# Kernel tuning notes

Measured on AMD Instinct MI355X. Metric: run time of the kernel, lower is better.

Reference implementation:

```python
import jax, jax.numpy as jnp
import numpy as np

B, S, DIN, DOUT, H = 4, 2048, 512, 512, 8
DH = DOUT // H
EPS = 1e-5


def _conv_bn(x, conv_w, conv_b, bn_gamma, bn_beta, bn_mean, bn_var):
    # x: [B, S, DIN] -> permute to [B, DIN, S] like torch
    xc = jnp.transpose(x, (0, 2, 1))
    y = jax.lax.conv_general_dilated(
        xc, conv_w, window_strides=(1,), padding=[(3, 3)],
        dimension_numbers=('NCH', 'OIH', 'NCH'))  # [B, DOUT, S]
    y = y + conv_b[None, :, None]
    # BatchNorm1d in eval mode: normalize per channel with running stats
    inv = jax.lax.rsqrt(bn_var + EPS)
    y = (y - bn_mean[None, :, None]) * (inv * bn_gamma)[None, :, None] + bn_beta[None, :, None]
    return jnp.transpose(y, (0, 2, 1))  # back to [B, S, DOUT]


def setup_inputs() -> dict:
    key = jax.random.key(0)
    ks = jax.random.split(key, 4)
    return {
        'q': jax.random.normal(ks[0], (B, S, DIN), dtype=jnp.float32),
        'k': jax.random.normal(ks[1], (B, S, DIN), dtype=jnp.float32),
        'v': jax.random.normal(ks[2], (B, S, DIN), dtype=jnp.float32),
        'conv_w': jax.random.normal(ks[3], (DOUT, DIN, 7), dtype=jnp.float32) * 0.02,
        'conv_b': jnp.zeros((DOUT,), jnp.float32),
        'bn_gamma': jnp.ones((DOUT,), jnp.float32),
        'bn_beta': jnp.zeros((DOUT,), jnp.float32),
        'bn_mean': jnp.zeros((DOUT,), jnp.float32),
        'bn_var': jnp.ones((DOUT,), jnp.float32),
        'ln_gamma': jnp.ones((DOUT,), jnp.float32),
        'ln_beta': jnp.zeros((DOUT,), jnp.float32),
    }


def reference(q, k, v, conv_w, conv_b, bn_gamma, bn_beta, bn_mean, bn_var,
              ln_gamma, ln_beta):
    # shared conv+BN preproc applied to q, k, v, then split into heads [B,S,H,DH]
    qh = _conv_bn(q, conv_w, conv_b, bn_gamma, bn_beta, bn_mean, bn_var).reshape(B, S, H, DH)
    kh = _conv_bn(k, conv_w, conv_b, bn_gamma, bn_beta, bn_mean, bn_var).reshape(B, S, H, DH)
    vh = _conv_bn(v, conv_w, conv_b, bn_gamma, bn_beta, bn_mean, bn_var).reshape(B, S, H, DH)
    # full QK^T score matrix, scaled, softmax, times V (mask is None)
    scores = jnp.einsum('bqhd,bkhd->bhqk', qh, kh) * (1.0 / np.sqrt(DH).astype(np.float32))
    probs = jax.nn.softmax(scores, axis=-1)
    out = jnp.einsum('bhqk,bkhd->bqhd', probs, vh).reshape(B, S, DOUT)
    # dropout(p=0) is identity; final LayerNorm over feature dim
    mu = jnp.mean(out, axis=-1, keepdims=True)
    var = jnp.mean(jnp.square(out - mu), axis=-1, keepdims=True)
    return (out - mu) * jax.lax.rsqrt(var + EPS) * ln_gamma + ln_beta
```

## Files before the change

kernel.cpp:

```cpp
#include <hip/hip_runtime.h>
#include <hip/hip_bf16.h>


#define B_ 4
#define S_ 2048
#define DIN_ 512
#define DOUT_ 512
#define H_ 8
#define DH_ 64
#define EPS_ 1e-5f
#define SP_ 2054

using bf16x8 = __attribute__((ext_vector_type(8))) short;
using f32x4  = __attribute__((ext_vector_type(4))) float;

__device__ __forceinline__ unsigned short f2bf(float x) {
    union { float f; unsigned u; } v; v.f = x;
    unsigned r = v.u + 0x7FFF + ((v.u >> 16) & 1);
    return (unsigned short)(r >> 16);
}

__device__ __forceinline__ unsigned cvt2(float lo, float hi) {
    unsigned r;
    asm("v_cvt_pk_bf16_f32 %0, %1, %2" : "=v"(r) : "v"(lo), "v"(hi));
    return r;
}

__device__ __forceinline__ float fexp2(float x) {
    float r;
    asm("v_exp_f32 %0, %1" : "=v"(r) : "v"(x));
    return r;
}

typedef __attribute__((address_space(1))) const unsigned int GU32;
typedef __attribute__((address_space(3))) unsigned int LU32;
__device__ __forceinline__ void gl_lds16(const void* g, void* l) {
    __builtin_amdgcn_global_load_lds((GU32*)g, (LU32*)l, 16, 0, 0);
}

__global__ void cast_x(const float* __restrict__ q, const float* __restrict__ k,
                       const float* __restrict__ v, unsigned short* __restrict__ xb) {
    int i = blockIdx.x * 256 + threadIdx.x;
    int row = i >> 6;
    int cin = (i & 63) * 8;
    int tb = row / SP_;
    int pr = row - tb * SP_;
    int tensor = tb >> 2;
    int b = tb & 3;
    unsigned short* dst = xb + (size_t)row * DIN_ + cin;
    if (pr < 3 || pr >= SP_ - 3) {
        *reinterpret_cast<uint4*>(dst) = make_uint4(0, 0, 0, 0);
    } else {
        const float* src = (tensor == 0 ? q : (tensor == 1 ? k : v)) +
                           ((size_t)b * S_ + (pr - 3)) * DIN_ + cin;
        float4 a0 = *reinterpret_cast<const float4*>(src);
        float4 a1 = *reinterpret_cast<const float4*>(src + 4);
        uint4 o;
        o.x = cvt2(a0.x, a0.y); o.y = cvt2(a0.z, a0.w);
        o.z = cvt2(a1.x, a1.y); o.w = cvt2(a1.z, a1.w);
        *reinterpret_cast<uint4*>(dst) = o;
    }
}

__global__ void prep_w(const float* __restrict__ w, const float* __restrict__ cb,
                       const float* __restrict__ gamma, const float* __restrict__ beta,
                       const float* __restrict__ mean, const float* __restrict__ var,
                       unsigned short* __restrict__ w_eff, float* __restrict__ b_eff) {
    int gid = blockIdx.x * blockDim.x + threadIdx.x;
    if (gid < DOUT_) {
        float sc = gamma[gid] * rsqrtf(var[gid] + EPS_);
        b_eff[gid] = (cb[gid] - mean[gid]) * sc + beta[gid];
    }
    int total = 7 * DOUT_ * DIN_;
    for (int i = gid; i < total; i += gridDim.x * blockDim.x) {
        int t = i / (DOUT_ * DIN_);
        int rem = i - t * (DOUT_ * DIN_);
        int co = rem >> 9;
        int ci = rem & 511;
        float sc = gamma[co] * rsqrtf(var[co] + EPS_);
        w_eff[i] = f2bf(w[(co * DIN_ + ci) * 7 + t] * sc);
    }
}

__global__ __launch_bounds__(256, 2) void conv_bn(
        const unsigned short* __restrict__ xb,
        const unsigned short* __restrict__ w_eff,
        const float* __restrict__ b_eff,
        unsigned short* __restrict__ out3) {
    __shared__ alignas(16) unsigned short As[2][192 * 32];
    __shared__ alignas(16) unsigned short Bs[3][256 * 32];

    int orig = blockIdx.x;
    int bid = (orig & 7) * 48 + (orig >> 3);
    int tensor = bid >> 7;
    int rem = bid & 127;
    int batch = rem >> 5;
    int stile = (rem >> 1) & 15;
    int cotile = rem & 1;
    int s0 = stile * 128;
    int co0 = cotile * 256;

    const unsigned short* xp = xb + (size_t)(tensor * 4 + batch) * SP_ * DIN_;
    unsigned short* out = out3 + (size_t)tensor * (B_ * S_ * DOUT_) +
                          (size_t)batch * S_ * DOUT_;

    const int tid = threadIdx.x;
    const int l = tid & 63;
    const int wv = tid >> 6;
    const int g = l >> 4;
    const int c16 = l & 15;
    const int wrow = (wv >> 1) * 64;
    const int wcol = (wv & 1) * 128;

    const int dr4 = l >> 2;
    const int sch = ((l & 3) ^ (dr4 & 3)) << 3;

#define STAGE_A(cc, buf) do {                                                   \
        _Pragma("unroll")                                                       \
        for (int j = 0; j < 3; ++j) {                                           \
            int r0 = (wv * 3 + j) * 16;                                         \
            int rs = r0 + dr4; if (rs > 133) rs = 133;                          \
            gl_lds16(xp + (size_t)(s0 + rs) * DIN_ + (cc) * 32 + sch,           \
                     &As[buf][r0 * 32]);                                        \
        }                                                                       \
    } while (0)

#define STAGE_B(cc, t, buf) do {                                                \
        const unsigned short* wp = w_eff + (size_t)(t) * (DOUT_ * DIN_) +       \
                                   (cc) * 32;                                   \
        _Pragma("unroll")                                                       \
        for (int j = 0; j < 4; ++j) {                                           \
            int r0 = (wv * 4 + j) * 16;                                         \
            gl_lds16(wp + (size_t)(co0 + r0 + dr4) * DIN_ + sch,                \
                     &Bs[buf][r0 * 32]);                                        \
        }                                                                       \
    } while (0)

    f32x4 acc[4][8] = {};

    STAGE_A(0, 0);
    STAGE_B(0, 0, 0);
    int bcur = 0;

    for (int cc = 0; cc < 16; ++cc) {
        const int ca = cc & 1;
        for (int t = 0; t < 7; ++t) {
            int bnext = bcur + 1; if (bnext == 3) bnext = 0;
            if (t < 6) {
                STAGE_B(cc, t + 1, bnext);
                asm volatile("s_waitcnt vmcnt(4)" ::: "memory");
            } else if (cc < 15) {
                STAGE_B(cc + 1, 0, bnext);
                STAGE_A(cc + 1, ca ^ 1);
                asm volatile("s_waitcnt vmcnt(7)" ::: "memory");
            } else {
                asm volatile("s_waitcnt vmcnt(0)" ::: "memory");
            }
            __builtin_amdgcn_s_barrier();

            const unsigned short* Ab = &As[ca][0];
            const unsigned short* Bb = &Bs[bcur][0];
            bf16x8 af[4], bfv[8];
#pragma unroll
            for (int m = 0; m < 4; ++m) {
                int r = wrow + m * 16 + c16 + t;
                af[m] = *reinterpret_cast<const bf16x8*>(
                    &Ab[r * 32 + ((g ^ (r & 3)) << 3)]);
            }
#pragma unroll
            for (int n = 0; n < 8; ++n) {
                int rb = wcol + n * 16 + c16;
                bfv[n] = *reinterpret_cast<const bf16x8*>(
                    &Bb[rb * 32 + ((g ^ (rb & 3)) << 3)]);
            }
            __builtin_amdgcn_s_setprio(1);
#pragma unroll
            for (int m = 0; m < 4; ++m)
#pragma unroll
                for (int n = 0; n < 8; ++n)
                    acc[m][n] = __builtin_amdgcn_mfma_f32_16x16x32_bf16(
                        af[m], bfv[n], acc[m][n], 0, 0, 0);
            __builtin_amdgcn_s_setprio(0);
            bcur = bnext;
        }
    }

    float osc = (tensor == 0) ? 0.125f * 1.44269504f : 1.0f;
#pragma unroll
    for (int m = 0; m < 4; ++m) {
        int rowb = s0 + wrow + m * 16 + 4 * g;
#pragma unroll
        for (int n = 0; n < 8; ++n) {
            int col = co0 + wcol + n * 16 + c16;
            float be = b_eff[col];
#pragma unroll
            for (int ri = 0; ri < 4; ++ri)
                out[(size_t)(rowb + ri) * DOUT_ + col] =
                    f2bf((acc[m][n][ri] + be) * osc);
        }
    }
#undef STAGE_A
#undef STAGE_B
}

__global__ void transpose_v(const unsigned short* __restrict__ vh,
                            unsigned short* __restrict__ vt) {
    __shared__ alignas(16) unsigned short T[64 * 64];
    int bid = blockIdx.x;
    int stile = bid & 31;
    int bh = bid >> 5;
    int b = bh >> 3;
    int h = bh & 7;
    int s0 = stile * 64;
    const unsigned short* src = vh + ((size_t)b * S_ + s0) * DOUT_ + h * DH_;
    unsigned short* dst = vt + (size_t)bh * DH_ * S_ + s0;
    int tid = threadIdx.x;
#pragma unroll
    for (int it = 0; it < 2; ++it) {
        int idx = tid + it * 256;
        int s = idx >> 3, dhc = idx & 7;
        uint4 val = *reinterpret_cast<const uint4*>(&src[(size_t)s * DOUT_ + dhc * 8]);
        *reinterpret_cast<uint4*>(&T[s * 64 + ((dhc ^ (s & 7) ^ ((s >> 3) & 7)) << 3)]) = val;
    }
    __syncthreads();
#pragma unroll
    for (int it = 0; it < 2; ++it) {
        int idx = tid + it * 256;
        int dh = idx >> 3, sc = idx & 7;
        unsigned short tmp[8];
#pragma unroll
        for (int j = 0; j < 8; ++j) {
            int s = sc * 8 + j;
            tmp[j] = T[s * 64 + (((dh >> 3) ^ (s & 7) ^ ((s >> 3) & 7)) << 3) + (dh & 7)];
        }
        *reinterpret_cast<uint4*>(&dst[(size_t)dh * S_ + sc * 8]) =
            *reinterpret_cast<const uint4*>(tmp);
    }
}

__global__ __launch_bounds__(256, 4) void attn(const unsigned short* __restrict__ qh,
                     const unsigned short* __restrict__ kh,
                     const unsigned short* __restrict__ vt,
                     float* __restrict__ out) {
    __shared__ alignas(16) unsigned short Ks[2][64 * 64];
    __shared__ alignas(16) unsigned short Vs[2][64 * 64];

    const int tid = threadIdx.x;
    const int l = tid & 63;
    const int wv = tid >> 6;
    const int g = l >> 4;
    const int c16 = l & 15;

    const int bid = blockIdx.x;
    const int qt = bid & 31;
    const int bh = bid >> 5;
    const int b = bh >> 3;
    const int h = bh & 7;
    const int s0 = qt * 64;

    const unsigned short* qp = qh + (size_t)b * S_ * DOUT_ + h * DH_;
    const unsigned short* kp = kh + (size_t)b * S_ * DOUT_ + h * DH_;
    const unsigned short* vp = vt + (size_t)bh * DH_ * S_;

    bf16x8 qf[2];
    {
        int row = s0 + wv * 16 + c16;
        qf[0] = *reinterpret_cast<const bf16x8*>(&qp[(size_t)row * DOUT_ + 8 * g]);
        qf[1] = *reinterpret_cast<const bf16x8*>(&qp[(size_t)row * DOUT_ + 32 + 8 * g]);
    }

    const int l3 = l >> 3;
    const int kchunk8 = ((l & 7) ^ l3) * 8;

#define STAGE(kt, buf) do {                                                          \
        const unsigned short* kgp = kp + (size_t)(kt) * 64 * DOUT_;                  \
        const unsigned short* vgp = vp + (size_t)(kt) * 64;                          \
        _Pragma("unroll")                                                            \
        for (int i = 0; i < 2; ++i) {                                                \
            int K0 = wv * 16 + i * 8;                                                \
            gl_lds16(kgp + (size_t)(K0 + l3) * DOUT_ + kchunk8, &Ks[buf][K0 * 64]);  \
            gl_lds16(vgp + (size_t)(K0 + l3) * S_   + kchunk8, &Vs[buf][K0 * 64]);   \
        }                                                                            \
    } while (0)

    f32x4 oacc[4] = {};
    float mrow = -1e30f, lrow = 0.f;

    const int sA = ((l & 16) << 1) | c16;
    const int sB = sA + 16;
    const bool hi = (l & 32) != 0;

    STAGE(0, 0);

    const int NT = S_ / 64;
    for (int kt = 0; kt < NT; ++kt) {
        const int cur = kt & 1;
        if (kt + 1 < NT) {
            STAGE(kt + 1, 1 - cur);
            asm volatile("s_waitcnt vmcnt(4)" ::: "memory");
        } else {
            asm volatile("s_waitcnt vmcnt(0)" ::: "memory");
        }
        __builtin_amdgcn_s_barrier();

        const char* KsB = (const char*)&Ks[cur][0];
        f32x4 sf[4] = {};
#pragma unroll
        for (int kk = 0; kk < 2; ++kk) {
            bf16x8 kf[4];
#pragma unroll
            for (int n = 0; n < 4; ++n)
                kf[n] = *reinterpret_cast<const bf16x8*>(
                    KsB + (n * 16 + c16) * 128 + (((4 * kk + g) ^ (l & 7)) << 4));
            __builtin_amdgcn_s_setprio(1);
#pragma unroll
            for (int n = 0; n < 4; ++n)
                sf[n] = __builtin_amdgcn_mfma_f32_16x16x32_bf16(kf[n], qf[kk], sf[n], 0, 0, 0);
            __builtin_amdgcn_s_setprio(0);
        }

        float t0 = fmaxf(fmaxf(sf[0][0], sf[0][1]), fmaxf(sf[0][2], sf[0][3]));
        float t1 = fmaxf(fmaxf(sf[1][0], sf[1][1]), fmaxf(sf[1][2], sf[1][3]));
        float t2 = fmaxf(fmaxf(sf[2][0], sf[2][1]), fmaxf(sf[2][2], sf[2][3]));
        float t3 = fmaxf(fmaxf(sf[3][0], sf[3][1]), fmaxf(sf[3][2], sf[3][3]));
        float m0 = fmaxf(fmaxf(t0, t1), fmaxf(t2, t3));
        m0 = fmaxf(m0, __shfl_xor(m0, 16, 64));
        m0 = fmaxf(m0, __shfl_xor(m0, 32, 64));
        if (!__all(m0 <= mrow + 8.f)) {
            float mnew = fmaxf(mrow, m0);
            float corr = fexp2(mrow - mnew);
            mrow = mnew;
            lrow *= corr;
#pragma unroll
            for (int n = 0; n < 4; ++n) {
                oacc[n][0] *= corr; oacc[n][1] *= corr;
                oacc[n][2] *= corr; oacc[n][3] *= corr;
            }
        }
        unsigned pk[4][2];
        float rsn[4];
#pragma unroll
        for (int n = 0; n < 4; ++n) {
            float p0 = fexp2(sf[n][0] - mrow);
            float p1 = fexp2(sf[n][1] - mrow);
            float p2 = fexp2(sf[n][2] - mrow);
            float p3 = fexp2(sf[n][3] - mrow);
            rsn[n] = (p0 + p1) + (p2 + p3);
            pk[n][0] = cvt2(p0, p1);
            pk[n][1] = cvt2(p2, p3);
        }
        float rs = (rsn[0] + rsn[1]) + (rsn[2] + rsn[3]);
        rs += __shfl_xor(rs, 16, 64);
        rs += __shfl_xor(rs, 32, 64);
        lrow += rs;

        const char* VsB = (const char*)&Vs[cur][0];
#pragma unroll
        for (int kk = 0; kk < 2; ++kk) {
            unsigned a0 = __shfl((int)pk[2 * kk][0], sA, 64);
            unsigned a1 = __shfl((int)pk[2 * kk][1], sA, 64);
            unsigned a2 = __shfl((int)pk[2 * kk][0], sB, 64);
            unsigned a3 = __shfl((int)pk[2 * kk][1], sB, 64);
            unsigned b0 = __shfl((int)pk[2 * kk + 1][0], sA, 64);
            unsigned b1 = __shfl((int)pk[2 * kk + 1][1], sA, 64);
            unsigned b2 = __shfl((int)pk[2 * kk + 1][0], sB, 64);
            unsigned b3 = __shfl((int)pk[2 * kk + 1][1], sB, 64);
            union { unsigned w[4]; bf16x8 v; } pu;
            pu.w[0] = hi ? b0 : a0;
            pu.w[1] = hi ? b1 : a1;
            pu.w[2] = hi ? b2 : a2;
            pu.w[3] = hi ? b3 : a3;
            bf16x8 vfr[4];
#pragma unroll
            for (int n = 0; n < 4; ++n)
                vfr[n] = *reinterpret_cast<const bf16x8*>(
                    VsB + (n * 16 + c16) * 128 + (((4 * kk + g) ^ (l & 7)) << 4));
            __builtin_amdgcn_s_setprio(1);
#pragma unroll
            for (int n = 0; n < 4; ++n)
                oacc[n] = __builtin_amdgcn_mfma_f32_16x16x32_bf16(vfr[n], pu.v, oacc[n], 0, 0, 0);
            __builtin_amdgcn_s_setprio(0);
        }
        __builtin_amdgcn_s_barrier();
    }

    {
        int row = s0 + wv * 16 + c16;
        float inv = 1.0f / lrow;
        float* op = out + (size_t)b * S_ * DOUT_ + h * DH_ + (size_t)row * DOUT_;
#pragma unroll
        for (int n = 0; n < 4; ++n) {
            f32x4 o = oacc[n];
            o[0] *= inv; o[1] *= inv; o[2] *= inv; o[3] *= inv;
            *reinterpret_cast<f32x4*>(&op[n * 16 + 4 * g]) = o;
        }
    }
#undef STAGE
}

__global__ void lnorm(float* __restrict__ out, const float* __restrict__ gamma,
                      const float* __restrict__ beta) {
    int tid = threadIdx.x;
    int lane = tid & 63;
    int wv = tid >> 6;
    int row = blockIdx.x * 4 + wv;
    float* p = out + (size_t)row * DOUT_;
    float4 v0 = *reinterpret_cast<const float4*>(&p[lane * 8]);
    float4 v1 = *reinterpret_cast<const float4*>(&p[lane * 8 + 4]);
    float s = v0.x + v0.y + v0.z + v0.w + v1.x + v1.y + v1.z + v1.w;
    float sq = v0.x * v0.x + v0.y * v0.y + v0.z * v0.z + v0.w * v0.w +
               v1.x * v1.x + v1.y * v1.y + v1.z * v1.z + v1.w * v1.w;
    for (int off = 1; off < 64; off <<= 1) {
        s += __shfl_xor(s, off, 64);
        sq += __shfl_xor(sq, off, 64);
    }
    float mu = s * (1.0f / 512.0f);
    float var = sq * (1.0f / 512.0f) - mu * mu;
    float rstd = rsqrtf(fmaxf(var, 0.f) + EPS_);
    float4 g0 = *reinterpret_cast<const float4*>(&gamma[lane * 8]);
    float4 g1 = *reinterpret_cast<const float4*>(&gamma[lane * 8 + 4]);
    float4 b0 = *reinterpret_cast<const float4*>(&beta[lane * 8]);
    float4 b1 = *reinterpret_cast<const float4*>(&beta[lane * 8 + 4]);
    float4 o0, o1;
    o0.x = (v0.x - mu) * rstd * g0.x + b0.x;
    o0.y = (v0.y - mu) * rstd * g0.y + b0.y;
    o0.z = (v0.z - mu) * rstd * g0.z + b0.z;
    o0.w = (v0.w - mu) * rstd * g0.w + b0.w;
    o1.x = (v1.x - mu) * rstd * g1.x + b1.x;
    o1.y = (v1.y - mu) * rstd * g1.y + b1.y;
    o1.z = (v1.z - mu) * rstd * g1.z + b1.z;
    o1.w = (v1.w - mu) * rstd * g1.w + b1.w;
    *reinterpret_cast<float4*>(&p[lane * 8]) = o0;
    *reinterpret_cast<float4*>(&p[lane * 8 + 4]) = o1;
}

extern "C" void kernel_launch(void* const* d_in, const int* in_sizes, int n_in,
                              void* d_out, int out_size, void* d_ws, size_t ws_size,
                              hipStream_t stream) {
    const float* q        = (const float*)d_in[0];
    const float* k        = (const float*)d_in[1];
    const float* v        = (const float*)d_in[2];
    const float* conv_w   = (const float*)d_in[3];
    const float* conv_b   = (const float*)d_in[4];
    const float* bn_gamma = (const float*)d_in[5];
    const float* bn_beta  = (const float*)d_in[6];
    const float* bn_mean  = (const float*)d_in[7];
    const float* bn_var   = (const float*)d_in[8];
    const float* ln_gamma = (const float*)d_in[9];
    const float* ln_beta  = (const float*)d_in[10];

    unsigned short* qh    = (unsigned short*)d_ws;
    unsigned short* kh    = qh + (size_t)B_ * S_ * DOUT_;
    unsigned short* vh    = kh + (size_t)B_ * S_ * DOUT_;
    unsigned short* w_eff = vh + (size_t)B_ * S_ * DOUT_;
    float* b_eff          = (float*)(w_eff + (size_t)7 * DOUT_ * DIN_);
    unsigned short* xb    = (unsigned short*)(b_eff + DOUT_);
    unsigned short* vt    = xb;

    float* out = (float*)d_out;

    cast_x<<<dim3(6162), dim3(256), 0, stream>>>(q, k, v, xb);
    prep_w<<<dim3(7168), dim3(256), 0, stream>>>(conv_w, conv_b, bn_gamma, bn_beta,
                                                 bn_mean, bn_var, w_eff, b_eff);
    conv_bn<<<dim3(384), dim3(256), 0, stream>>>(xb, w_eff, b_eff, qh);
    transpose_v<<<dim3(1024), dim3(256), 0, stream>>>(vh, vt);
    attn<<<dim3(1024), dim3(256), 0, stream>>>(qh, kh, vt, out);
    lnorm<<<dim3(2048), dim3(256), 0, stream>>>(out, ln_gamma, ln_beta);
}
```

Measured before the change: 188.0 us.

## Restructure conv GEMM to 64-row tiles with register-loaded A and more blocks

The conv_bn kernel tile changes from 128x256 to 64x256 per block, doubling the grid to 768 blocks, and the launch-bounds occupancy target rises from 2 to 3. The A (input) operand no longer goes through shared memory. Each wave loads it straight from global memory into registers per tap, double-buffered across an unrolled phase loop, while B keeps its triple-buffered LDS pipeline with a changed swizzle. The aim is better CU fill and less LDS traffic and pressure. In exchange, A gets reloaded from global or cache for every one of the 7 taps, and each block reuses B over fewer rows.

```diff
diff --git a/kernel.cpp b/kernel.cpp
--- a/kernel.cpp
+++ b/kernel.cpp
@@ -82,22 +82,22 @@
     }
 }
 
-__global__ __launch_bounds__(256, 2) void conv_bn(
+__global__ __launch_bounds__(256, 3) void conv_bn(
         const unsigned short* __restrict__ xb,
         const unsigned short* __restrict__ w_eff,
         const float* __restrict__ b_eff,
         unsigned short* __restrict__ out3) {
-    __shared__ alignas(16) unsigned short As[2][192 * 32];
     __shared__ alignas(16) unsigned short Bs[3][256 * 32];
 
     int orig = blockIdx.x;
-    int bid = (orig & 7) * 48 + (orig >> 3);
-    int tensor = bid >> 7;
-    int rem = bid & 127;
-    int batch = rem >> 5;
-    int stile = (rem >> 1) & 15;
-    int cotile = rem & 1;
-    int s0 = stile * 128;
+    int bid = (orig & 7) * 96 + (orig >> 3);
+    int tensor = bid >> 8;
+    int rem = bid & 255;
+    int batch = rem >> 6;
+    int rem2 = rem & 63;
+    int stile = rem2 >> 1;
+    int cotile = rem2 & 1;
+    int s0 = stile * 64;
     int co0 = cotile * 256;
 
     const unsigned short* xp = xb + (size_t)(tensor * 4 + batch) * SP_ * DIN_;
@@ -109,21 +109,9 @@
     const int wv = tid >> 6;
     const int g = l >> 4;
     const int c16 = l & 15;
-    const int wrow = (wv >> 1) * 64;
-    const int wcol = (wv & 1) * 128;
 
     const int dr4 = l >> 2;
-    const int sch = ((l & 3) ^ (dr4 & 3)) << 3;
-
-#define STAGE_A(cc, buf) do {                                                   \
-        _Pragma("unroll")                                                       \
-        for (int j = 0; j < 3; ++j) {                                           \
-            int r0 = (wv * 3 + j) * 16;                                         \
-            int rs = r0 + dr4; if (rs > 133) rs = 133;                          \
-            gl_lds16(xp + (size_t)(s0 + rs) * DIN_ + (cc) * 32 + sch,           \
-                     &As[buf][r0 * 32]);                                        \
-        }                                                                       \
-    } while (0)
+    const int sch = ((l & 3) ^ ((l >> 3) & 3)) << 3;
 
 #define STAGE_B(cc, t, buf) do {                                                \
         const unsigned short* wp = w_eff + (size_t)(t) * (DOUT_ * DIN_) +       \
@@ -136,62 +124,68 @@
         }                                                                       \
     } while (0)
 
-    f32x4 acc[4][8] = {};
-
-    STAGE_A(0, 0);
+#define LOAD_A(cc, t, AF) do {                                                  \
+        _Pragma("unroll")                                                       \
+        for (int m = 0; m < 4; ++m)                                             \
+            AF[m] = *reinterpret_cast<const uint4*>(                            \
+                xp + (size_t)(s0 + m * 16 + c16 + (t)) * DIN_ + (cc) * 32 + 8 * g); \
+    } while (0)
+
+#define COMPUTE(AF, buf) do {                                                   \
+        bf16x8 bfv[4];                                                          \
+        _Pragma("unroll")                                                       \
+        for (int n = 0; n < 4; ++n) {                                           \
+            int rb = wv * 64 + n * 16 + c16;                                    \
+            bfv[n] = *reinterpret_cast<const bf16x8*>(                          \
+                &Bs[buf][rb * 32 + ((g ^ ((rb >> 1) & 3)) << 3)]);              \
+        }                                                                       \
+        __builtin_amdgcn_s_setprio(1);                                          \
+        _Pragma("unroll")                                                       \
+        for (int m = 0; m < 4; ++m) {                                           \
+            bf16x8 am = *reinterpret_cast<const bf16x8*>(&AF[m]);               \
+            _Pragma("unroll")                                                   \
+            for (int n = 0; n < 4; ++n)                                         \
+                acc[m][n] = __builtin_amdgcn_mfma_f32_16x16x32_bf16(            \
+                    am, bfv[n], acc[m][n], 0, 0, 0);                            \
+        }                                                                       \
+        __builtin_amdgcn_s_setprio(0);                                          \
+    } while (0)
+
+#define PHASE(CUR, NXT) do {                                                    \
+        int tn = t + 1, ccn = cc;                                               \
+        if (tn == 7) { tn = 0; ccn = cc + 1; }                                  \
+        int bnext = (bcur == 2) ? 0 : bcur + 1;                                 \
+        if (ccn < 16) {                                                         \
+            STAGE_B(ccn, tn, bnext);                                            \
+            LOAD_A(ccn, tn, NXT);                                               \
+            asm volatile("s_waitcnt vmcnt(8)" ::: "memory");                    \
+        } else {                                                                \
+            asm volatile("s_waitcnt vmcnt(0)" ::: "memory");                    \
+        }                                                                       \
+        __builtin_amdgcn_s_barrier();                                           \
+        COMPUTE(CUR, bcur);                                                     \
+        bcur = bnext; t = tn; cc = ccn;                                         \
+    } while (0)
+
+    f32x4 acc[4][4] = {};
+    uint4 afA[4], afB[4];
+
     STAGE_B(0, 0, 0);
-    int bcur = 0;
-
-    for (int cc = 0; cc < 16; ++cc) {
-        const int ca = cc & 1;
-        for (int t = 0; t < 7; ++t) {
-            int bnext = bcur + 1; if (bnext == 3) bnext = 0;
-            if (t < 6) {
-                STAGE_B(cc, t + 1, bnext);
-                asm volatile("s_waitcnt vmcnt(4)" ::: "memory");
-            } else if (cc < 15) {
-                STAGE_B(cc + 1, 0, bnext);
-                STAGE_A(cc + 1, ca ^ 1);
-                asm volatile("s_waitcnt vmcnt(7)" ::: "memory");
-            } else {
-                asm volatile("s_waitcnt vmcnt(0)" ::: "memory");
-            }
-            __builtin_amdgcn_s_barrier();
-
-            const unsigned short* Ab = &As[ca][0];
-            const unsigned short* Bb = &Bs[bcur][0];
-            bf16x8 af[4], bfv[8];
-#pragma unroll
-            for (int m = 0; m < 4; ++m) {
-                int r = wrow + m * 16 + c16 + t;
-                af[m] = *reinterpret_cast<const bf16x8*>(
-                    &Ab[r * 32 + ((g ^ (r & 3)) << 3)]);
-            }
-#pragma unroll
-            for (int n = 0; n < 8; ++n) {
-                int rb = wcol + n * 16 + c16;
-                bfv[n] = *reinterpret_cast<const bf16x8*>(
-                    &Bb[rb * 32 + ((g ^ (rb & 3)) << 3)]);
-            }
-            __builtin_amdgcn_s_setprio(1);
-#pragma unroll
-            for (int m = 0; m < 4; ++m)
-#pragma unroll
-                for (int n = 0; n < 8; ++n)
-                    acc[m][n] = __builtin_amdgcn_mfma_f32_16x16x32_bf16(
-                        af[m], bfv[n], acc[m][n], 0, 0, 0);
-            __builtin_amdgcn_s_setprio(0);
-            bcur = bnext;
-        }
+    LOAD_A(0, 0, afA);
+    int bcur = 0, cc = 0, t = 0;
+
+    for (int p = 0; p < 112; p += 2) {
+        PHASE(afA, afB);
+        PHASE(afB, afA);
     }
 
     float osc = (tensor == 0) ? 0.125f * 1.44269504f : 1.0f;
 #pragma unroll
     for (int m = 0; m < 4; ++m) {
-        int rowb = s0 + wrow + m * 16 + 4 * g;
-#pragma unroll
-        for (int n = 0; n < 8; ++n) {
-            int col = co0 + wcol + n * 16 + c16;
+        int rowb = s0 + m * 16 + 4 * g;
+#pragma unroll
+        for (int n = 0; n < 4; ++n) {
+            int col = co0 + wv * 64 + n * 16 + c16;
             float be = b_eff[col];
 #pragma unroll
             for (int ri = 0; ri < 4; ++ri)
@@ -199,8 +193,10 @@
                     f2bf((acc[m][n][ri] + be) * osc);
         }
     }
-#undef STAGE_A
 #undef STAGE_B
+#undef LOAD_A
+#undef COMPUTE
+#undef PHASE
 }
 
 __global__ void transpose_v(const unsigned short* __restrict__ vh,
@@ -462,7 +458,7 @@
     cast_x<<<dim3(6162), dim3(256), 0, stream>>>(q, k, v, xb);
     prep_w<<<dim3(7168), dim3(256), 0, stream>>>(conv_w, conv_b, bn_gamma, bn_beta,
                                                  bn_mean, bn_var, w_eff, b_eff);
-    conv_bn<<<dim3(384), dim3(256), 0, stream>>>(xb, w_eff, b_eff, qh);
+    conv_bn<<<dim3(768), dim3(256), 0, stream>>>(xb, w_eff, b_eff, qh);
     transpose_v<<<dim3(1024), dim3(256), 0, stream>>>(vh, vt);
     attn<<<dim3(1024), dim3(256), 0, stream>>>(qh, kh, vt, out);
     lnorm<<<dim3(2048), dim3(256), 0, stream>>>(out, ln_gamma, ln_beta);
```

Result: slower. 299.8 us (+59.4%).
